# Kernel tuning notes

Hardware: AMD Instinct MI355X
Metric: run time of the kernel (lower is better)

Reference implementation:

```python
import jax, jax.numpy as jnp
import numpy as np

DMODEL = 1024
NHEAD = 16
HDIM = DMODEL // NHEAD
CTXLEN = 2048
BATCH = 2


def setup_inputs() -> dict:
    key = jax.random.key(0)
    k_x, k_qkv, k_pw, k_pb = jax.random.split(key, 4)
    x = jax.random.normal(k_x, (BATCH, CTXLEN, DMODEL), dtype=jnp.float32)
    # nn.Linear weights: stored as [out, in]; init scale ~ 1/sqrt(in)
    s = 1.0 / np.sqrt(DMODEL)
    w_qkv = jax.random.uniform(k_qkv, (3 * DMODEL, DMODEL), minval=-s, maxval=s, dtype=jnp.float32)
    w_proj = jax.random.uniform(k_pw, (DMODEL, DMODEL), minval=-s, maxval=s, dtype=jnp.float32)
    b_proj = jax.random.uniform(k_pb, (DMODEL,), minval=-s, maxval=s, dtype=jnp.float32)
    return {"x": x, "w_qkv": w_qkv, "w_proj": w_proj, "b_proj": b_proj}


def reference(x, w_qkv, w_proj, b_proj):
    b, t, c = x.shape
    qkv = jnp.einsum('btc,oc->bto', x, w_qkv)  # [b, t, 3c]
    q, k, v = jnp.split(qkv, 3, axis=-1)
    # [b, nhead, t, hdim]
    q = q.reshape(b, t, NHEAD, HDIM).transpose(0, 2, 1, 3)
    k = k.reshape(b, t, NHEAD, HDIM).transpose(0, 2, 1, 3)
    v = v.reshape(b, t, NHEAD, HDIM).transpose(0, 2, 1, 3)
    # NOTE: original code MULTIPLIES by sqrt(hdim) (not the usual divide)
    att = jnp.einsum('bhqd,bhkd->bhqk', q, k) * (HDIM ** 0.5)
    causal = jnp.tril(jnp.ones((t, t), dtype=bool))  # [t, t]
    att = jnp.where(causal[None, None], att, -jnp.inf)
    att = jax.nn.softmax(att, axis=-1)
    y = jnp.einsum('bhqk,bhkd->bhqd', att, v)
    y = y.transpose(0, 2, 1, 3).reshape(b, t, c)
    return jnp.einsum('btc,oc->bto', y, w_proj) + b_proj
```

## Files before the change

kernel.cpp:

```cpp
#include <hip/hip_runtime.h>
#include <hip/hip_bf16.h>

#define DMODEL 1024
#define NHEAD 16
#define HDIM 64
#define CTXLEN 2048
#define BATCH 2
#define M_TOTAL (BATCH * CTXLEN)

typedef unsigned short ushort_t;
typedef __attribute__((ext_vector_type(8))) _Float16 f16x8;
typedef __attribute__((ext_vector_type(8))) unsigned short u16x8;
typedef __attribute__((ext_vector_type(4))) float f32x4;
typedef __attribute__((ext_vector_type(4))) unsigned short u16x4;

__device__ __forceinline__ unsigned short f32_f16(float f) {
    return __builtin_bit_cast(unsigned short, (_Float16)f);
}
__device__ __forceinline__ float f16_f32(unsigned short h) {
    return (float)__builtin_bit_cast(_Float16, h);
}
__device__ __forceinline__ float fast_exp2(float x) {
    return __builtin_amdgcn_exp2f(x);
}
__device__ __forceinline__ f32x4 mfma16f(f16x8 a, f16x8 b, f32x4 c) {
    return __builtin_amdgcn_mfma_f32_16x16x32_f16(a, b, c, 0, 0, 0);
}
__device__ __forceinline__ void gload_lds16(const ushort_t* g, ushort_t* l) {
    __builtin_amdgcn_global_load_lds(
        (const __attribute__((address_space(1))) void*)g,
        (__attribute__((address_space(3))) void*)l, 16, 0, 0);
}
__device__ __forceinline__ int unit_off(int qt) {
    if (qt < 8)  return qt;
    if (qt < 16) return 8 + (qt - 8) * 2;
    if (qt < 24) return 24 + (qt - 16) * 3;
    return 48 + (qt - 24) * 4;
}

__global__ __launch_bounds__(256)
void conv_f32_f16(const float* __restrict__ src, ushort_t* __restrict__ dst, int n4) {
    for (int i = blockIdx.x * blockDim.x + threadIdx.x; i < n4;
         i += gridDim.x * blockDim.x) {
        const float4 v = reinterpret_cast<const float4*>(src)[i];
        u16x4 o;
        o[0] = f32_f16(v.x); o[1] = f32_f16(v.y);
        o[2] = f32_f16(v.z); o[3] = f32_f16(v.w);
        reinterpret_cast<u16x4*>(dst)[i] = o;
    }
}

template<bool QKV_EPI>
__global__ __launch_bounds__(256)
void gemm_f16_nt(const ushort_t* __restrict__ A, const ushort_t* __restrict__ B,
                 const float* __restrict__ bias, float* __restrict__ C,
                 ushort_t* __restrict__ qf, ushort_t* __restrict__ kf,
                 ushort_t* __restrict__ vb,
                 int M, int N, int K) {
    __shared__ ushort_t lds[2 * 4096];

    const int tid  = threadIdx.x;
    const int lane = tid & 63;
    const int wave = tid >> 6;
    const int lc   = lane & 15;
    const int lg   = lane >> 4;
    const int wr   = wave >> 1;
    const int wc   = wave & 1;
    const int row0 = blockIdx.y * 128;
    const int col0 = blockIdx.x * 128;

    const int c0 = tid, c1 = 256 + tid;
    const int r0 = c0 >> 2, l0 = (c0 & 3) ^ ((c0 >> 3) & 3);
    const int r1 = c1 >> 2, l1 = (c1 & 3) ^ ((c1 >> 3) & 3);
    const size_t gaoff0 = (size_t)(row0 + r0) * K + l0 * 8;
    const size_t gaoff1 = (size_t)(row0 + r1) * K + l1 * 8;
    const size_t gboff0 = (size_t)(col0 + r0) * K + l0 * 8;
    const size_t gboff1 = (size_t)(col0 + r1) * K + l1 * 8;
    const int ld0 = c0 * 8, ld1 = c1 * 8;

    int aoff[4], boff[4];
    #pragma unroll
    for (int m = 0; m < 4; ++m) {
        const int ra = wr * 64 + m * 16 + lc;
        aoff[m] = ra * 32 + ((lg ^ ((ra >> 1) & 3)) * 8);
        const int rb = wc * 64 + m * 16 + lc;
        boff[m] = rb * 32 + ((lg ^ ((rb >> 1) & 3)) * 8);
    }

    f32x4 acc[4][4];
    const f32x4 zero4 = {0.f, 0.f, 0.f, 0.f};
    #pragma unroll
    for (int m = 0; m < 4; ++m)
        #pragma unroll
        for (int n = 0; n < 4; ++n) acc[m][n] = zero4;

    const int NT = K >> 5;

    auto stage = [&](int kt) {
        const int ko = kt * 32;
        gload_lds16(A + gaoff0 + ko, &lds[ld0]);
        gload_lds16(A + gaoff1 + ko, &lds[ld1]);
        gload_lds16(B + gboff0 + ko, &lds[4096 + ld0]);
        gload_lds16(B + gboff1 + ko, &lds[4096 + ld1]);
    };

    stage(0);
    for (int kt = 0; kt < NT; ++kt) {
        __syncthreads();
        f16x8 fa[4], fb[4];
        #pragma unroll
        for (int m = 0; m < 4; ++m) {
            fa[m] = *reinterpret_cast<const f16x8*>(&lds[aoff[m]]);
            fb[m] = *reinterpret_cast<const f16x8*>(&lds[4096 + boff[m]]);
        }
        __syncthreads();
        if (kt + 1 < NT) stage(kt + 1);
        #pragma unroll
        for (int m = 0; m < 4; ++m)
            #pragma unroll
            for (int n = 0; n < 4; ++n)
                acc[m][n] = mfma16f(fa[m], fb[n], acc[m][n]);
    }

    if (!QKV_EPI) {
        #pragma unroll
        for (int m = 0; m < 4; ++m)
            #pragma unroll
            for (int i = 0; i < 4; ++i) {
                const int r = row0 + wr * 64 + m * 16 + lg * 4 + i;
                #pragma unroll
                for (int n = 0; n < 4; ++n) {
                    const int c = col0 + wc * 64 + n * 16 + lc;
                    C[(size_t)r * N + c] = acc[m][n][i] + bias[c];
                }
            }
    } else {
        #pragma unroll
        for (int m = 0; m < 4; ++m)
            #pragma unroll
            for (int i = 0; i < 4; ++i) {
                const int r = row0 + wr * 64 + m * 16 + lg * 4 + i;
                const int bb = r >> 11;
                const int t  = r & 2047;
                #pragma unroll
                for (int n = 0; n < 4; ++n) {
                    const int cg  = col0 + wc * 64 + n * 16 + lc;
                    const int sec = cg >> 10;
                    const int ch  = cg & 1023;
                    const int hh  = ch >> 6;
                    const int d   = ch & 63;
                    const size_t off = (((size_t)(bb * NHEAD + hh)) * CTXLEN + t) * HDIM + d;
                    const unsigned short hv = f32_f16(acc[m][n][i]);
                    if (sec == 0)      qf[off] = hv;
                    else if (sec == 1) kf[off] = hv;
                    else               vb[off] = hv;
                }
            }
    }
}

__global__ __launch_bounds__(256)
void transpose_v(const ushort_t* __restrict__ vb, ushort_t* __restrict__ vt) {
    __shared__ ushort_t T[64][66];
    const int tt = blockIdx.x;
    const int bh = blockIdx.y;
    const int tid = threadIdx.x;
    const int r  = tid >> 2;
    const int c0 = (tid & 3) * 16;

    const ushort_t* src = vb + ((size_t)bh * CTXLEN + tt * 64) * HDIM;
    #pragma unroll
    for (int half = 0; half < 2; ++half) {
        const u16x8 v = *reinterpret_cast<const u16x8*>(&src[(size_t)r * HDIM + c0 + half * 8]);
        #pragma unroll
        for (int j = 0; j < 8; ++j) T[r][c0 + half * 8 + j] = v[j];
    }
    __syncthreads();
    ushort_t* dst = vt + ((size_t)bh * HDIM + r) * CTXLEN + tt * 64 + c0;
    u16x8 o0, o1;
    #pragma unroll
    for (int j = 0; j < 8; ++j) { o0[j] = T[c0 + j][r]; o1[j] = T[c0 + 8 + j][r]; }
    *reinterpret_cast<u16x8*>(&dst[0]) = o0;
    *reinterpret_cast<u16x8*>(&dst[8]) = o1;
}

#define SCALE_LOG2 11.5415603271f

__global__ __launch_bounds__(256)
void attn_fwd7(const ushort_t* __restrict__ qf, const ushort_t* __restrict__ kf,
               const ushort_t* __restrict__ vt,
               ushort_t* __restrict__ py, float* __restrict__ pml) {
    __shared__ ushort_t KH[2][4096];
    __shared__ ushort_t VT[2][4096];
    __shared__ ushort_t Ps[4][16][64];

    const int id    = blockIdx.x;
    const int bh    = id & 31;
    const int u_off = id >> 5;
    int qt, u;
    if (u_off < 8)       { qt = u_off;                          u = 0; }
    else if (u_off < 24) { const int t = u_off - 8;  qt = 8  + (t >> 1); u = t & 1; }
    else if (u_off < 48) { const int t = u_off - 24; const int q3 = t / 3; qt = 16 + q3; u = t - q3 * 3; }
    else                 { const int t = u_off - 48; qt = 24 + (t >> 2); u = t & 3; }
    const int total = qt + 1;
    const int nu    = (qt >> 3) + 1;
    const int base  = total / nu, rem = total % nu;
    const int kb0   = u * base + (u < rem ? u : rem);
    const int len   = base + (u < rem ? 1 : 0);
    const int slot  = bh * 80 + u_off;

    const int tid  = threadIdx.x;
    const int wave = tid >> 6;
    const int lane = tid & 63;
    const int lc   = lane & 15;
    const int lg   = lane >> 4;

    const ushort_t* kfb = kf + (size_t)bh * CTXLEN * HDIM;
    const ushort_t* vtb = vt + (size_t)bh * HDIM * CTXLEN;

    const int cA = tid, cB = 256 + tid;
    const int rA = cA >> 3, sgA = (cA & 7) ^ (rA & 7);
    const int rB = cB >> 3, sgB = (cB & 7) ^ (rB & 7);

    auto stage = [&](int kb, int buf) {
        const size_t koff = (size_t)(kb * 64);
        gload_lds16(kfb + (koff + rA) * HDIM + sgA * 8, &KH[buf][cA * 8]);
        gload_lds16(kfb + (koff + rB) * HDIM + sgB * 8, &KH[buf][cB * 8]);
        gload_lds16(vtb + (size_t)rA * CTXLEN + kb * 64 + sgA * 8, &VT[buf][cA * 8]);
        gload_lds16(vtb + (size_t)rB * CTXLEN + kb * 64 + sgB * 8, &VT[buf][cB * 8]);
    };

    const size_t qrow = (size_t)bh * CTXLEN + qt * 64 + wave * 16 + lc;
    f16x8 qfr[2];
    #pragma unroll
    for (int ds = 0; ds < 2; ++ds)
        qfr[ds] = *reinterpret_cast<const f16x8*>(&qf[qrow * HDIM + ds * 32 + lg * 8]);

    const f32x4 zero4 = {0.f, 0.f, 0.f, 0.f};
    f32x4 yacc[4];
    #pragma unroll
    for (int t = 0; t < 4; ++t) yacc[t] = zero4;
    float m_i = -1e30f, l_i = 0.f;

    stage(kb0, 0);
    __syncthreads();

    int cur = 0;
    for (int s = 0; s < len; ++s) {
        const int kb = kb0 + s;
        if (s + 1 < len) stage(kb + 1, cur ^ 1);

        f16x8 kfr[4][2];
        #pragma unroll
        for (int tc = 0; tc < 4; ++tc) {
            const int rk = tc * 16 + lc;
            #pragma unroll
            for (int ds = 0; ds < 2; ++ds) {
                const int a = rk * 64 + (((ds * 4 + lg) ^ (rk & 7)) * 8);
                kfr[tc][ds] = *reinterpret_cast<const f16x8*>(&KH[cur][a]);
            }
        }
        f16x8 vf[4][2];
        #pragma unroll
        for (int t = 0; t < 4; ++t) {
            const int rv = t * 16 + lc;
            #pragma unroll
            for (int ks = 0; ks < 2; ++ks) {
                const int a = rv * 64 + (((ks * 4 + lg) ^ (rv & 7)) * 8);
                vf[t][ks] = *reinterpret_cast<const f16x8*>(&VT[cur][a]);
            }
        }

        f32x4 sacc[4];
        #pragma unroll
        for (int tc = 0; tc < 4; ++tc) sacc[tc] = zero4;
        __builtin_amdgcn_s_setprio(1);
        #pragma unroll
        for (int tc = 0; tc < 4; ++tc)
            #pragma unroll
            for (int ds = 0; ds < 2; ++ds)
                sacc[tc] = mfma16f(kfr[tc][ds], qfr[ds], sacc[tc]);
        __builtin_amdgcn_s_setprio(0);

        const bool diag = (kb == qt);
        const int q_loc = wave * 16 + lc;
        float p[4][4];
        #pragma unroll
        for (int tc = 0; tc < 4; ++tc)
            #pragma unroll
            for (int i = 0; i < 4; ++i) {
                float uu = sacc[tc][i] * SCALE_LOG2;
                if (diag && (tc * 16 + lg * 4 + i) > q_loc) uu = -1e30f;
                p[tc][i] = uu;
            }
        float mx = p[0][0];
        #pragma unroll
        for (int tc = 0; tc < 4; ++tc)
            #pragma unroll
            for (int i = 0; i < 4; ++i) mx = fmaxf(mx, p[tc][i]);
        mx = fmaxf(mx, __shfl_xor(mx, 16));
        mx = fmaxf(mx, __shfl_xor(mx, 32));
        const float mnew = fmaxf(m_i, mx);
        const float corr = fast_exp2(m_i - mnew);
        float psum = 0.f;
        #pragma unroll
        for (int tc = 0; tc < 4; ++tc)
            #pragma unroll
            for (int i = 0; i < 4; ++i) {
                const float e = fast_exp2(p[tc][i] - mnew);
                p[tc][i] = e;
                psum += e;
            }
        psum += __shfl_xor(psum, 16);
        psum += __shfl_xor(psum, 32);
        l_i = l_i * corr + psum;
        m_i = mnew;
        #pragma unroll
        for (int t = 0; t < 4; ++t) yacc[t] *= corr;

        #pragma unroll
        for (int tc = 0; tc < 4; ++tc) {
            const int eb = tc * 16 + lg * 4;
            const int se = ((((eb >> 3) ^ (lc & 7)) << 3) | (eb & 7));
            u16x4 pk;
            #pragma unroll
            for (int i = 0; i < 4; ++i) pk[i] = f32_f16(p[tc][i]);
            *reinterpret_cast<u16x4*>(&Ps[wave][lc][se]) = pk;
        }
        f16x8 pa[2];
        #pragma unroll
        for (int ks = 0; ks < 2; ++ks) {
            const int sl = ((ks * 4 + lg) ^ (lc & 7)) << 3;
            pa[ks] = *reinterpret_cast<const f16x8*>(&Ps[wave][lc][sl]);
        }
        __builtin_amdgcn_s_setprio(1);
        #pragma unroll
        for (int t = 0; t < 4; ++t)
            #pragma unroll
            for (int ks = 0; ks < 2; ++ks)
                yacc[t] = mfma16f(vf[t][ks], pa[ks], yacc[t]);
        __builtin_amdgcn_s_setprio(0);

        __syncthreads();
        cur ^= 1;
    }

    const int row = wave * 16 + lc;
    ushort_t* prow = py + ((size_t)slot * 64 + row) * 64;
    #pragma unroll
    for (int t = 0; t < 4; ++t) {
        u16x4 o;
        #pragma unroll
        for (int i = 0; i < 4; ++i) o[i] = f32_f16(yacc[t][i]);
        *reinterpret_cast<u16x4*>(&prow[t * 16 + lg * 4]) = o;
    }
    if (lg == 0) {
        pml[(size_t)slot * 128 + row]      = m_i;
        pml[(size_t)slot * 128 + 64 + row] = l_i;
    }
}

__global__ __launch_bounds__(256)
void merge_attn(const ushort_t* __restrict__ py, const float* __restrict__ pml,
                ushort_t* __restrict__ yb) {
    const int bid = blockIdx.x;
    const int bh  = bid >> 5;
    const int qt  = bid & 31;
    const int b   = bh >> 4;
    const int h   = bh & 15;
    const int tid = threadIdx.x;
    const int row = tid >> 2;
    const int d0  = (tid & 3) * 16;

    const int nu    = (qt >> 3) + 1;
    const int sbase = bh * 80 + unit_off(qt);

    float mu[4], lu[4];
    float M = -1e30f;
    #pragma unroll
    for (int u = 0; u < 4; ++u) {
        if (u < nu) {
            mu[u] = pml[(size_t)(sbase + u) * 128 + row];
            lu[u] = pml[(size_t)(sbase + u) * 128 + 64 + row];
            M = fmaxf(M, mu[u]);
        } else { mu[u] = -1e30f; lu[u] = 0.f; }
    }
    float w[4], ltot = 0.f;
    #pragma unroll
    for (int u = 0; u < 4; ++u) {
        w[u] = (u < nu) ? fast_exp2(mu[u] - M) : 0.f;
        ltot += w[u] * lu[u];
    }

    float y[16];
    #pragma unroll
    for (int j = 0; j < 16; ++j) y[j] = 0.f;
    #pragma unroll
    for (int u = 0; u < 4; ++u) {
        if (u < nu) {
            const ushort_t* pr = py + ((size_t)(sbase + u) * 64 + row) * 64 + d0;
            const u16x8 a = *reinterpret_cast<const u16x8*>(&pr[0]);
            const u16x8 c = *reinterpret_cast<const u16x8*>(&pr[8]);
            #pragma unroll
            for (int j = 0; j < 8; ++j) {
                y[j]     += w[u] * f16_f32(a[j]);
                y[8 + j] += w[u] * f16_f32(c[j]);
            }
        }
    }
    const float inv = 1.0f / ltot;
    ushort_t* dst = yb + (size_t)(b * CTXLEN + qt * 64 + row) * DMODEL + h * HDIM + d0;
    u16x8 o0, o1;
    #pragma unroll
    for (int j = 0; j < 8; ++j) {
        o0[j] = f32_f16(y[j] * inv);
        o1[j] = f32_f16(y[8 + j] * inv);
    }
    *reinterpret_cast<u16x8*>(&dst[0]) = o0;
    *reinterpret_cast<u16x8*>(&dst[8]) = o1;
}

extern "C" void kernel_launch(void* const* d_in, const int* in_sizes, int n_in,
                              void* d_out, int out_size, void* d_ws, size_t ws_size,
                              hipStream_t stream) {
    const float* x      = (const float*)d_in[0];
    const float* w_qkv  = (const float*)d_in[1];
    const float* w_proj = (const float*)d_in[2];
    const float* b_proj = (const float*)d_in[3];
    float* out = (float*)d_out;

    char* ws = (char*)d_ws;
    ushort_t* wqf = (ushort_t*)(ws);
    ushort_t* wpf = (ushort_t*)(ws + 6291456);
    ushort_t* xf  = (ushort_t*)(ws + 8388608);
    ushort_t* qf  = (ushort_t*)(ws + 16777216);
    ushort_t* kf  = (ushort_t*)(ws + 25165824);
    ushort_t* vb  = (ushort_t*)(ws + 33554432);
    ushort_t* vt  = (ushort_t*)(ws + 41943040);
    ushort_t* py  = (ushort_t*)(ws + 50331648);
    float*    pml = (float*)   (ws + 71303168);
    ushort_t* yb  = xf;

    const dim3 blk(256);

    conv_f32_f16<<<dim3(2048), blk, 0, stream>>>(x, xf, M_TOTAL * DMODEL / 4);
    conv_f32_f16<<<dim3(2048), blk, 0, stream>>>(w_qkv, wqf, 3 * DMODEL * DMODEL / 4);
    conv_f32_f16<<<dim3(1024), blk, 0, stream>>>(w_proj, wpf, DMODEL * DMODEL / 4);

    gemm_f16_nt<true><<<dim3(3 * DMODEL / 128, M_TOTAL / 128), blk, 0, stream>>>(
        xf, wqf, nullptr, nullptr, qf, kf, vb, M_TOTAL, 3 * DMODEL, DMODEL);

    transpose_v<<<dim3(CTXLEN / 64, BATCH * NHEAD), blk, 0, stream>>>(vb, vt);

    attn_fwd7<<<dim3(2560), blk, 0, stream>>>(qf, kf, vt, py, pml);
    merge_attn<<<dim3(1024), blk, 0, stream>>>(py, pml, yb);

    gemm_f16_nt<false><<<dim3(DMODEL / 128, M_TOTAL / 128), blk, 0, stream>>>(
        yb, wpf, b_proj, out, nullptr, nullptr, nullptr, M_TOTAL, DMODEL, DMODEL);
}
```

Before: 126.9 us.

## Fuse conversion kernels, narrow projection GEMM tile, add lazy softmax rescale

Three separate changes. The three f32-to-f16 conversion launches become one kernel that walks all three buffers. The output projection GEMM is templated on tile width and launched with 64-wide column tiles, doubling its block count to fill more compute units. The attention online softmax skips the max update and accumulator rescale when the new block max exceeds the running max by at most 8 in log2 units, which saves exp and multiply work but lets unnormalised values grow up to 256x in fp16 P.

```diff
diff --git a/kernel.cpp b/kernel.cpp
--- a/kernel.cpp
+++ b/kernel.cpp
@@ -39,25 +39,34 @@
 }
 
 __global__ __launch_bounds__(256)
-void conv_f32_f16(const float* __restrict__ src, ushort_t* __restrict__ dst, int n4) {
-    for (int i = blockIdx.x * blockDim.x + threadIdx.x; i < n4;
+void conv3_f32_f16(const float* __restrict__ a, ushort_t* __restrict__ da, int na4,
+                   const float* __restrict__ b, ushort_t* __restrict__ db, int nb4,
+                   const float* __restrict__ c, ushort_t* __restrict__ dc, int nc4) {
+    const int n = na4 + nb4 + nc4;
+    for (int i = blockIdx.x * blockDim.x + threadIdx.x; i < n;
          i += gridDim.x * blockDim.x) {
-        const float4 v = reinterpret_cast<const float4*>(src)[i];
+        const float* s; ushort_t* d; int j = i;
+        if (j < na4) { s = a; d = da; }
+        else if (j - na4 < nb4) { j -= na4; s = b; d = db; }
+        else { j -= na4 + nb4; s = c; d = dc; }
+        const float4 v = reinterpret_cast<const float4*>(s)[j];
         u16x4 o;
         o[0] = f32_f16(v.x); o[1] = f32_f16(v.y);
         o[2] = f32_f16(v.z); o[3] = f32_f16(v.w);
-        reinterpret_cast<u16x4*>(dst)[i] = o;
-    }
-}
-
-template<bool QKV_EPI>
+        reinterpret_cast<u16x4*>(d)[j] = o;
+    }
+}
+
+template<int BN, bool QKV_EPI>
 __global__ __launch_bounds__(256)
 void gemm_f16_nt(const ushort_t* __restrict__ A, const ushort_t* __restrict__ B,
                  const float* __restrict__ bias, float* __restrict__ C,
                  ushort_t* __restrict__ qf, ushort_t* __restrict__ kf,
                  ushort_t* __restrict__ vb,
                  int M, int N, int K) {
-    __shared__ ushort_t lds[2 * 4096];
+    constexpr int NF = BN / 32;
+    constexpr int BOFF = 4096;
+    __shared__ ushort_t lds[BOFF + BN * 32];
 
     const int tid  = threadIdx.x;
     const int lane = tid & 63;
@@ -67,7 +76,7 @@
     const int wr   = wave >> 1;
     const int wc   = wave & 1;
     const int row0 = blockIdx.y * 128;
-    const int col0 = blockIdx.x * 128;
+    const int col0 = blockIdx.x * BN;
 
     const int c0 = tid, c1 = 256 + tid;
     const int r0 = c0 >> 2, l0 = (c0 & 3) ^ ((c0 >> 3) & 3);
@@ -78,21 +87,24 @@
     const size_t gboff1 = (size_t)(col0 + r1) * K + l1 * 8;
     const int ld0 = c0 * 8, ld1 = c1 * 8;
 
-    int aoff[4], boff[4];
+    int aoff[4], boff[NF];
     #pragma unroll
     for (int m = 0; m < 4; ++m) {
         const int ra = wr * 64 + m * 16 + lc;
         aoff[m] = ra * 32 + ((lg ^ ((ra >> 1) & 3)) * 8);
-        const int rb = wc * 64 + m * 16 + lc;
-        boff[m] = rb * 32 + ((lg ^ ((rb >> 1) & 3)) * 8);
-    }
-
-    f32x4 acc[4][4];
+    }
+    #pragma unroll
+    for (int n = 0; n < NF; ++n) {
+        const int rb = wc * (NF * 16) + n * 16 + lc;
+        boff[n] = rb * 32 + ((lg ^ ((rb >> 1) & 3)) * 8);
+    }
+
+    f32x4 acc[4][NF];
     const f32x4 zero4 = {0.f, 0.f, 0.f, 0.f};
     #pragma unroll
     for (int m = 0; m < 4; ++m)
         #pragma unroll
-        for (int n = 0; n < 4; ++n) acc[m][n] = zero4;
+        for (int n = 0; n < NF; ++n) acc[m][n] = zero4;
 
     const int NT = K >> 5;
 
@@ -100,25 +112,26 @@
         const int ko = kt * 32;
         gload_lds16(A + gaoff0 + ko, &lds[ld0]);
         gload_lds16(A + gaoff1 + ko, &lds[ld1]);
-        gload_lds16(B + gboff0 + ko, &lds[4096 + ld0]);
-        gload_lds16(B + gboff1 + ko, &lds[4096 + ld1]);
+        gload_lds16(B + gboff0 + ko, &lds[BOFF + ld0]);
+        if (BN == 128) gload_lds16(B + gboff1 + ko, &lds[BOFF + ld1]);
     };
 
     stage(0);
     for (int kt = 0; kt < NT; ++kt) {
         __syncthreads();
-        f16x8 fa[4], fb[4];
-        #pragma unroll
-        for (int m = 0; m < 4; ++m) {
+        f16x8 fa[4], fb[NF];
+        #pragma unroll
+        for (int m = 0; m < 4; ++m)
             fa[m] = *reinterpret_cast<const f16x8*>(&lds[aoff[m]]);
-            fb[m] = *reinterpret_cast<const f16x8*>(&lds[4096 + boff[m]]);
-        }
+        #pragma unroll
+        for (int n = 0; n < NF; ++n)
+            fb[n] = *reinterpret_cast<const f16x8*>(&lds[BOFF + boff[n]]);
         __syncthreads();
         if (kt + 1 < NT) stage(kt + 1);
         #pragma unroll
         for (int m = 0; m < 4; ++m)
             #pragma unroll
-            for (int n = 0; n < 4; ++n)
+            for (int n = 0; n < NF; ++n)
                 acc[m][n] = mfma16f(fa[m], fb[n], acc[m][n]);
     }
 
@@ -129,8 +142,8 @@
             for (int i = 0; i < 4; ++i) {
                 const int r = row0 + wr * 64 + m * 16 + lg * 4 + i;
                 #pragma unroll
-                for (int n = 0; n < 4; ++n) {
-                    const int c = col0 + wc * 64 + n * 16 + lc;
+                for (int n = 0; n < NF; ++n) {
+                    const int c = col0 + wc * (NF * 16) + n * 16 + lc;
                     C[(size_t)r * N + c] = acc[m][n][i] + bias[c];
                 }
             }
@@ -143,8 +156,8 @@
                 const int bb = r >> 11;
                 const int t  = r & 2047;
                 #pragma unroll
-                for (int n = 0; n < 4; ++n) {
-                    const int cg  = col0 + wc * 64 + n * 16 + lc;
+                for (int n = 0; n < NF; ++n) {
+                    const int cg  = col0 + wc * (NF * 16) + n * 16 + lc;
                     const int sec = cg >> 10;
                     const int ch  = cg & 1023;
                     const int hh  = ch >> 6;
@@ -300,23 +313,39 @@
             for (int i = 0; i < 4; ++i) mx = fmaxf(mx, p[tc][i]);
         mx = fmaxf(mx, __shfl_xor(mx, 16));
         mx = fmaxf(mx, __shfl_xor(mx, 32));
-        const float mnew = fmaxf(m_i, mx);
-        const float corr = fast_exp2(m_i - mnew);
-        float psum = 0.f;
-        #pragma unroll
-        for (int tc = 0; tc < 4; ++tc)
-            #pragma unroll
-            for (int i = 0; i < 4; ++i) {
-                const float e = fast_exp2(p[tc][i] - mnew);
-                p[tc][i] = e;
-                psum += e;
-            }
-        psum += __shfl_xor(psum, 16);
-        psum += __shfl_xor(psum, 32);
-        l_i = l_i * corr + psum;
-        m_i = mnew;
-        #pragma unroll
-        for (int t = 0; t < 4; ++t) yacc[t] *= corr;
+
+        if (__all(mx <= m_i + 8.0f)) {
+            float psum = 0.f;
+            #pragma unroll
+            for (int tc = 0; tc < 4; ++tc)
+                #pragma unroll
+                for (int i = 0; i < 4; ++i) {
+                    const float e = fast_exp2(p[tc][i] - m_i);
+                    p[tc][i] = e;
+                    psum += e;
+                }
+            psum += __shfl_xor(psum, 16);
+            psum += __shfl_xor(psum, 32);
+            l_i += psum;
+        } else {
+            const float mnew = fmaxf(m_i, mx);
+            const float corr = fast_exp2(m_i - mnew);
+            float psum = 0.f;
+            #pragma unroll
+            for (int tc = 0; tc < 4; ++tc)
+                #pragma unroll
+                for (int i = 0; i < 4; ++i) {
+                    const float e = fast_exp2(p[tc][i] - mnew);
+                    p[tc][i] = e;
+                    psum += e;
+                }
+            psum += __shfl_xor(psum, 16);
+            psum += __shfl_xor(psum, 32);
+            l_i = l_i * corr + psum;
+            m_i = mnew;
+            #pragma unroll
+            for (int t = 0; t < 4; ++t) yacc[t] *= corr;
+        }
 
         #pragma unroll
         for (int tc = 0; tc < 4; ++tc) {
@@ -443,11 +472,12 @@
 
     const dim3 blk(256);
 
-    conv_f32_f16<<<dim3(2048), blk, 0, stream>>>(x, xf, M_TOTAL * DMODEL / 4);
-    conv_f32_f16<<<dim3(2048), blk, 0, stream>>>(w_qkv, wqf, 3 * DMODEL * DMODEL / 4);
-    conv_f32_f16<<<dim3(1024), blk, 0, stream>>>(w_proj, wpf, DMODEL * DMODEL / 4);
-
-    gemm_f16_nt<true><<<dim3(3 * DMODEL / 128, M_TOTAL / 128), blk, 0, stream>>>(
+    conv3_f32_f16<<<dim3(2048), blk, 0, stream>>>(
+        x, xf, M_TOTAL * DMODEL / 4,
+        w_qkv, wqf, 3 * DMODEL * DMODEL / 4,
+        w_proj, wpf, DMODEL * DMODEL / 4);
+
+    gemm_f16_nt<128, true><<<dim3(3 * DMODEL / 128, M_TOTAL / 128), blk, 0, stream>>>(
         xf, wqf, nullptr, nullptr, qf, kf, vb, M_TOTAL, 3 * DMODEL, DMODEL);
 
     transpose_v<<<dim3(CTXLEN / 64, BATCH * NHEAD), blk, 0, stream>>>(vb, vt);
@@ -455,6 +485,6 @@
     attn_fwd7<<<dim3(2560), blk, 0, stream>>>(qf, kf, vt, py, pml);
     merge_attn<<<dim3(1024), blk, 0, stream>>>(py, pml, yb);
 
-    gemm_f16_nt<false><<<dim3(DMODEL / 128, M_TOTAL / 128), blk, 0, stream>>>(
+    gemm_f16_nt<64, false><<<dim3(DMODEL / 64, M_TOTAL / 128), blk, 0, stream>>>(
         yb, wpf, b_proj, out, nullptr, nullptr, nullptr, M_TOTAL, DMODEL, DMODEL);
 }
```

Result: faster. 120.9 us (-4.7%).
